# Kernel optimization log

Hardware: AMD Instinct MI355X
Metric: run time of the kernel (lower is better)

## Reference

```python
import jax, jax.numpy as jnp
import numpy as np

B = 256      # number of graphs
IN = 128     # input_dim
FD = 256     # feature_dim (dims[1])
HID = 256    # hidden_dim of attention block (dims[2])
OUT = 128    # final output dim (dims[3])
TXT = 512    # text_emb_dim

LENGTHS = np.asarray(128 + (np.arange(B) % 256), dtype=np.int64)  # ragged lens 128..383
N = int(LENGTHS.sum())  # 65408 total nodes
LMAX = int(LENGTHS.max())  # 383


def setup_inputs() -> dict:
    key = jax.random.key(0)
    ks = jax.random.split(key, 16)
    s = 0.02
    return {
        "input": jax.random.normal(ks[0], (N, IN), jnp.float32),
        "text_emb": jax.random.normal(ks[1], (B, TXT), jnp.float32),
        "repeat_list": jnp.asarray(LENGTHS),
        # layer 0: Linear(IN -> FD)
        "W0": jax.random.normal(ks[2], (IN, FD), jnp.float32) * s,
        "b0": jax.random.normal(ks[3], (FD,), jnp.float32) * s,
        # cross-attention block params
        "Wq": jax.random.normal(ks[4], (TXT, FD), jnp.float32) * s,
        "bq": jax.random.normal(ks[5], (FD,), jnp.float32) * s,
        "Wk": jax.random.normal(ks[6], (FD, FD), jnp.float32) * s,
        "bk": jax.random.normal(ks[7], (FD,), jnp.float32) * s,
        "Wv": jax.random.normal(ks[8], (FD, FD), jnp.float32) * s,
        "bv": jax.random.normal(ks[9], (FD,), jnp.float32) * s,
        "Wo": jax.random.normal(ks[10], (FD, HID), jnp.float32) * s,
        "bo": jax.random.normal(ks[11], (HID,), jnp.float32) * s,
        # layer 2: Linear(HID -> OUT), last layer (no activation)
        "W2": jax.random.normal(ks[12], (HID, OUT), jnp.float32) * s,
        "b2": jax.random.normal(ks[13], (OUT,), jnp.float32) * s,
    }


def _cross_attention(h, text_emb, repeat_list, Wq, bq, Wk, bk, Wv, bv, Wo, bo):
    # h: [N, FD] packed ragged node features; repeat_list: [B] lengths (constant ints)
    n = h.shape[0]
    b = repeat_list.shape[0]
    fd = h.shape[1]
    # pad ragged -> [B, LMAX, FD] (pad value 0) + validity mask
    seg = jnp.repeat(jnp.arange(b), repeat_list, total_repeat_length=n)  # [N] graph id
    offsets = jnp.cumsum(repeat_list) - repeat_list                      # [B] start of each graph
    pos = jnp.arange(n) - offsets[seg]                                   # [N] within-graph pos
    padded = jnp.zeros((b, LMAX, fd), h.dtype).at[seg, pos].set(h)
    valid = jnp.arange(LMAX)[None, :] < repeat_list[:, None]             # [B, L]

    q = text_emb @ Wq + bq                              # [B, FD]
    k = (padded @ Wk + bk) * valid[..., None]           # masked_fill(mask==0, 0)
    v = (padded @ Wv + bv) * valid[..., None]

    # query is broadcast identically over the padded-length axis, so each row of the
    # [L, L] score matrix is the same vector: scores[b, j] = q[b] . k[b, j]
    scores = jnp.einsum('bf,bjf->bj', q, k)             # [B, L]
    scores = jnp.where(valid, scores, -jnp.inf)         # mask invalid columns j
    p = jax.nn.softmax(scores, axis=-1)                 # [B, L]
    # output = attention^T @ value with identical rows => out[b,j,:] = p[b,j] * sum_i v[b,i,:]
    v_sum = v.sum(axis=1)                               # [B, FD] (padded rows already zero)
    out_pad = p[..., None] * v_sum[:, None, :]          # [B, L, FD]
    out_nodes = out_pad[seg, pos]                       # unpad-concat -> [N, FD]
    return out_nodes @ Wo + bo                          # [N, HID]


def reference(input, text_emb, repeat_list, W0, b0, Wq, bq, Wk, bk, Wv, bv, Wo, bo, W2, b2):
    h = jax.nn.relu(input @ W0 + b0)                                     # layer 0 + relu
    h = _cross_attention(h, text_emb, repeat_list, Wq, bq, Wk, bk, Wv, bv, Wo, bo)
    h = jax.nn.relu(h)                                                   # layer 1 + relu
    return h @ W2 + b2                                                   # layer 2 (last, no act)
```

## Files before the change

kernel.cpp:

```cpp
#include <hip/hip_runtime.h>
#include <math.h>

#define B_G   256
#define IN_D  128
#define FD    256
#define HID   256
#define OUT_D 128
#define TXT   512

typedef short bf16x8 __attribute__((ext_vector_type(8)));
typedef float f32x4  __attribute__((ext_vector_type(4)));

#define WPAD 40

__device__ __forceinline__ unsigned bf_rne(float x) {
    unsigned u = __float_as_uint(x);
    u += 0x7fffu + ((u >> 16) & 1u);
    return u >> 16;
}
__device__ __forceinline__ float bf_to_f(unsigned h) {
    return __uint_as_float(h << 16);
}
__device__ __forceinline__ void split2(float a0, float a1, unsigned& hp, unsigned& lp) {
    unsigned h0 = bf_rne(a0), h1 = bf_rne(a1);
    float r0 = a0 - bf_to_f(h0), r1 = a1 - bf_to_f(h1);
    hp = h0 | (bf_rne(a1) << 16);
    lp = bf_rne(r0) | (bf_rne(r1) << 16);
    (void)h1;
}

__global__ __launch_bounds__(256) void k_wsplit(
    const float* __restrict__ W0, const float* __restrict__ W2,
    unsigned short* __restrict__ W0sH, unsigned short* __restrict__ W0sL,
    unsigned short* __restrict__ W2sH, unsigned short* __restrict__ W2sL)
{
    int t = blockIdx.x * 256 + threadIdx.x;
    if (t < 1024) {
        int kc = t >> 8, c = t & 255;
        size_t base = (size_t)(kc * 256 + c) * WPAD;
        for (int kk = 0; kk < 32; kk++) {
            float v = W0[(size_t)(kc * 32 + kk) * FD + c];
            unsigned h = bf_rne(v);
            float r = v - bf_to_f(h);
            W0sH[base + kk] = (unsigned short)h;
            W0sL[base + kk] = (unsigned short)bf_rne(r);
        }
    } else {
        int e = t - 1024;
        int kc = e >> 7, c = e & 127;
        size_t base = (size_t)(kc * 128 + c) * WPAD;
        for (int kk = 0; kk < 32; kk++) {
            float v = W2[(size_t)(kc * 32 + kk) * OUT_D + c];
            unsigned h = bf_rne(v);
            float r = v - bf_to_f(h);
            W2sH[base + kk] = (unsigned short)h;
            W2sL[base + kk] = (unsigned short)bf_rne(r);
        }
    }
}

__global__ __launch_bounds__(256) void k_prep(
    const float* __restrict__ text_emb, const float* __restrict__ Wq,
    const float* __restrict__ bq, const float* __restrict__ Wk,
    const int* __restrict__ lens, float* __restrict__ qk,
    int* __restrict__ offsets)
{
    int b = blockIdx.x, t = threadIdx.x;
    __shared__ float te[TXT];
    __shared__ float q[FD];
    for (int i = t; i < TXT; i += 256) te[i] = text_emb[(size_t)b * TXT + i];
    __syncthreads();
    float acc = bq[t];
    for (int k = 0; k < TXT; k++) acc = fmaf(te[k], Wq[k * FD + t], acc);
    q[t] = acc;
    __syncthreads();
    float a2 = 0.f;
    for (int f = 0; f < FD; f++) a2 = fmaf(Wk[t * FD + f], q[f], a2);
    qk[b * FD + t] = a2;
    if (b == 0 && t == 0) {
        int off = 0;
        for (int i = 0; i < B_G; i++) { offsets[i] = off; off += lens[i]; }
        offsets[B_G] = off;
    }
}

__global__ __launch_bounds__(256, 2) void k_l0_mfma(
    const float* __restrict__ X,
    const unsigned short* __restrict__ W0sH, const unsigned short* __restrict__ W0sL,
    const float* __restrict__ b0, const float* __restrict__ qk,
    const int* __restrict__ offsets,
    float* __restrict__ scores, float* __restrict__ hsum)
{
    int b = blockIdx.y;
    int off = offsets[b], len = offsets[b + 1] - off;
    int n0 = blockIdx.x * 64;
    if (n0 >= len) return;
    int nvalid = min(64, len - n0);

    __shared__ __align__(16) unsigned short XsH[64 * WPAD], XsL[64 * WPAD];
    __shared__ __align__(16) unsigned short WsH[256 * WPAD], WsL[256 * WPAD];
    __shared__ float qks[FD];
    __shared__ float bsh[FD];

    int tid = threadIdx.x;
    int lane = tid & 63, w = tid >> 6;
    int ln = lane & 15, quad = lane >> 4;

    qks[tid] = qk[b * FD + tid];
    bsh[tid] = b0[tid];

    f32x4 acc[4][4] = {};

    const float* Xg = X + (size_t)(off + n0) * IN_D;
    int node_s = tid >> 2, koff = (tid & 3) * 8;

    for (int kc = 0; kc < 4; kc++) {
        float xv[8];
        if (node_s < nvalid) {
            const float4* src = (const float4*)(Xg + (size_t)node_s * IN_D + kc * 32 + koff);
            float4 v0 = src[0], v1 = src[1];
            xv[0] = v0.x; xv[1] = v0.y; xv[2] = v0.z; xv[3] = v0.w;
            xv[4] = v1.x; xv[5] = v1.y; xv[6] = v1.z; xv[7] = v1.w;
        } else {
#pragma unroll
            for (int q = 0; q < 8; q++) xv[q] = 0.f;
        }
        uint4 hq, lq;
        split2(xv[0], xv[1], hq.x, lq.x);
        split2(xv[2], xv[3], hq.y, lq.y);
        split2(xv[4], xv[5], hq.z, lq.z);
        split2(xv[6], xv[7], hq.w, lq.w);
        *(uint4*)&XsH[node_s * WPAD + koff] = hq;
        *(uint4*)&XsL[node_s * WPAD + koff] = lq;

        {
            const uint4* gh = (const uint4*)(W0sH + (size_t)kc * 256 * WPAD);
            const uint4* gl = (const uint4*)(W0sL + (size_t)kc * 256 * WPAD);
            uint4* lh = (uint4*)WsH;
            uint4* ll = (uint4*)WsL;
#pragma unroll
            for (int r = 0; r < 5; r++) {
                lh[tid + 256 * r] = gh[tid + 256 * r];
                ll[tid + 256 * r] = gl[tid + 256 * r];
            }
        }
        __syncthreads();

        bf16x8 AH[4], AL[4], BH[4], BL[4];
#pragma unroll
        for (int i = 0; i < 4; i++) {
            AH[i] = *(const bf16x8*)&XsH[(16 * i + ln) * WPAD + quad * 8];
            AL[i] = *(const bf16x8*)&XsL[(16 * i + ln) * WPAD + quad * 8];
        }
#pragma unroll
        for (int j = 0; j < 4; j++) {
            int c = 64 * w + 16 * j + ln;
            BH[j] = *(const bf16x8*)&WsH[c * WPAD + quad * 8];
            BL[j] = *(const bf16x8*)&WsL[c * WPAD + quad * 8];
        }
#pragma unroll
        for (int i = 0; i < 4; i++)
#pragma unroll
            for (int j = 0; j < 4; j++) {
                acc[i][j] = __builtin_amdgcn_mfma_f32_16x16x32_bf16(AH[i], BH[j], acc[i][j], 0, 0, 0);
                acc[i][j] = __builtin_amdgcn_mfma_f32_16x16x32_bf16(AH[i], BL[j], acc[i][j], 0, 0, 0);
                acc[i][j] = __builtin_amdgcn_mfma_f32_16x16x32_bf16(AL[i], BH[j], acc[i][j], 0, 0, 0);
            }
        __syncthreads();
    }

    float sp[4][4];
    float cs[4] = {0.f, 0.f, 0.f, 0.f};
#pragma unroll
    for (int i = 0; i < 4; i++)
#pragma unroll
        for (int r = 0; r < 4; r++) sp[i][r] = 0.f;

#pragma unroll
    for (int i = 0; i < 4; i++)
#pragma unroll
        for (int j = 0; j < 4; j++) {
            int c = 64 * w + 16 * j + ln;
            float bb = bsh[c], qv = qks[c];
#pragma unroll
            for (int r = 0; r < 4; r++) {
                int node = 16 * i + 4 * quad + r;
                float h = acc[i][j][r] + bb;
                h = (h > 0.f && node < nvalid) ? h : 0.f;
                sp[i][r] = fmaf(h, qv, sp[i][r]);
                cs[j] += h;
            }
        }
#pragma unroll
    for (int i = 0; i < 4; i++)
#pragma unroll
        for (int r = 0; r < 4; r++) {
            float s = sp[i][r];
            s += __shfl_xor(s, 1); s += __shfl_xor(s, 2);
            s += __shfl_xor(s, 4); s += __shfl_xor(s, 8);
            sp[i][r] = s;
        }
    if (ln == 0) {
#pragma unroll
        for (int i = 0; i < 4; i++)
#pragma unroll
            for (int r = 0; r < 4; r++) {
                int node = 16 * i + 4 * quad + r;
                if (node < nvalid) atomicAdd(&scores[off + n0 + node], sp[i][r]);
            }
    }
#pragma unroll
    for (int j = 0; j < 4; j++) {
        float s = cs[j];
        s += __shfl_xor(s, 16); s += __shfl_xor(s, 32);
        if (quad == 0) atomicAdd(&hsum[b * FD + 64 * w + 16 * j + ln], s);
    }
}

__global__ __launch_bounds__(256) void k_graph(
    const float* __restrict__ scores, const float* __restrict__ hsum,
    const float* __restrict__ Wv, const float* __restrict__ bv,
    const float* __restrict__ Wo, const int* __restrict__ offsets,
    float* __restrict__ wvec, float* __restrict__ smax, float* __restrict__ dinv)
{
    int b = blockIdx.x, t = threadIdx.x;
    int off = offsets[b], len = offsets[b + 1] - off;
    __shared__ float redm[4];
    __shared__ float reds[4];
    __shared__ float hs[FD];
    __shared__ float vs[FD];

    float m = -INFINITY;
    for (int i = t; i < len; i += 256) m = fmaxf(m, scores[off + i]);
    for (int d = 1; d < 64; d <<= 1) m = fmaxf(m, __shfl_xor(m, d));
    if ((t & 63) == 0) redm[t >> 6] = m;
    __syncthreads();
    m = fmaxf(fmaxf(redm[0], redm[1]), fmaxf(redm[2], redm[3]));

    float s = 0.f;
    for (int i = t; i < len; i += 256) s += expf(scores[off + i] - m);
    for (int d = 1; d < 64; d <<= 1) s += __shfl_xor(s, d);
    if ((t & 63) == 0) reds[t >> 6] = s;
    hs[t] = hsum[b * FD + t];
    __syncthreads();
    s = reds[0] + reds[1] + reds[2] + reds[3];

    float v = bv[t] * (float)len;
    for (int f = 0; f < FD; f++) v = fmaf(hs[f], Wv[f * FD + t], v);
    vs[t] = v;
    __syncthreads();
    float w = 0.f;
    for (int f = 0; f < FD; f++) w = fmaf(vs[f], Wo[f * HID + t], w);
    wvec[b * HID + t] = w;
    if (t == 0) { smax[b] = m; dinv[b] = 1.0f / s; }
}

__global__ __launch_bounds__(256, 2) void k_fin_mfma(
    const float* __restrict__ scores, const float* __restrict__ wvec,
    const float* __restrict__ bo,
    const unsigned short* __restrict__ W2sH, const unsigned short* __restrict__ W2sL,
    const float* __restrict__ b2, const float* __restrict__ smax,
    const float* __restrict__ dinv, const int* __restrict__ offsets,
    float* __restrict__ Y)
{
    int b = blockIdx.y;
    int off = offsets[b], len = offsets[b + 1] - off;
    int n0 = blockIdx.x * 64;
    if (n0 >= len) return;
    int nvalid = min(64, len - n0);

    int tid = threadIdx.x;
    int lane = tid & 63, w = tid >> 6;
    int ln = lane & 15, quad = lane >> 4;

    __shared__ __align__(16) unsigned short ZsH[64 * WPAD], ZsL[64 * WPAD];
    __shared__ __align__(16) unsigned short WsH[128 * WPAD], WsL[128 * WPAD];
    __shared__ float ps[64];
    __shared__ float wsh[HID];
    __shared__ float bosh[HID];
    __shared__ float b2sh[OUT_D];

    wsh[tid] = wvec[b * HID + tid];
    bosh[tid] = bo[tid];
    if (tid < OUT_D) b2sh[tid] = b2[tid];
    if (tid < 64) {
        float p = 0.f;
        if (tid < nvalid) p = expf(scores[off + n0 + tid] - smax[b]) * dinv[b];
        ps[tid] = p;
    }
    __syncthreads();

    f32x4 acc[4][2] = {};
    int node_s = tid >> 2, koff = (tid & 3) * 8;
    float pn = ps[node_s];

    for (int kc = 0; kc < 8; kc++) {
        {
            int kb = kc * 32 + koff;
            uint4 hq, lq;
            float z0, z1;
            z0 = fmaxf(fmaf(pn, wsh[kb + 0], bosh[kb + 0]), 0.f);
            z1 = fmaxf(fmaf(pn, wsh[kb + 1], bosh[kb + 1]), 0.f);
            split2(z0, z1, hq.x, lq.x);
            z0 = fmaxf(fmaf(pn, wsh[kb + 2], bosh[kb + 2]), 0.f);
            z1 = fmaxf(fmaf(pn, wsh[kb + 3], bosh[kb + 3]), 0.f);
            split2(z0, z1, hq.y, lq.y);
            z0 = fmaxf(fmaf(pn, wsh[kb + 4], bosh[kb + 4]), 0.f);
            z1 = fmaxf(fmaf(pn, wsh[kb + 5], bosh[kb + 5]), 0.f);
            split2(z0, z1, hq.z, lq.z);
            z0 = fmaxf(fmaf(pn, wsh[kb + 6], bosh[kb + 6]), 0.f);
            z1 = fmaxf(fmaf(pn, wsh[kb + 7], bosh[kb + 7]), 0.f);
            split2(z0, z1, hq.w, lq.w);
            *(uint4*)&ZsH[node_s * WPAD + koff] = hq;
            *(uint4*)&ZsL[node_s * WPAD + koff] = lq;
        }
        {
            const uint4* gh = (const uint4*)(W2sH + (size_t)kc * 128 * WPAD);
            const uint4* gl = (const uint4*)(W2sL + (size_t)kc * 128 * WPAD);
            uint4* lh = (uint4*)WsH;
            uint4* ll = (uint4*)WsL;
            lh[tid] = gh[tid];          ll[tid] = gl[tid];
            lh[tid + 256] = gh[tid + 256]; ll[tid + 256] = gl[tid + 256];
            if (tid < 128) { lh[tid + 512] = gh[tid + 512]; ll[tid + 512] = gl[tid + 512]; }
        }
        __syncthreads();

        bf16x8 AH[4], AL[4], BH[2], BL[2];
#pragma unroll
        for (int i = 0; i < 4; i++) {
            AH[i] = *(const bf16x8*)&ZsH[(16 * i + ln) * WPAD + quad * 8];
            AL[i] = *(const bf16x8*)&ZsL[(16 * i + ln) * WPAD + quad * 8];
        }
#pragma unroll
        for (int j = 0; j < 2; j++) {
            int c = 32 * w + 16 * j + ln;
            BH[j] = *(const bf16x8*)&WsH[c * WPAD + quad * 8];
            BL[j] = *(const bf16x8*)&WsL[c * WPAD + quad * 8];
        }
#pragma unroll
        for (int i = 0; i < 4; i++)
#pragma unroll
            for (int j = 0; j < 2; j++) {
                acc[i][j] = __builtin_amdgcn_mfma_f32_16x16x32_bf16(AH[i], BH[j], acc[i][j], 0, 0, 0);
                acc[i][j] = __builtin_amdgcn_mfma_f32_16x16x32_bf16(AH[i], BL[j], acc[i][j], 0, 0, 0);
                acc[i][j] = __builtin_amdgcn_mfma_f32_16x16x32_bf16(AL[i], BH[j], acc[i][j], 0, 0, 0);
            }
        __syncthreads();
    }

#pragma unroll
    for (int i = 0; i < 4; i++)
#pragma unroll
        for (int j = 0; j < 2; j++) {
            int c = 32 * w + 16 * j + ln;
            float bb = b2sh[c];
#pragma unroll
            for (int r = 0; r < 4; r++) {
                int node = 16 * i + 4 * quad + r;
                if (node < nvalid)
                    Y[(size_t)(off + n0 + node) * OUT_D + c] = acc[i][j][r] + bb;
            }
        }
}

extern "C" void kernel_launch(void* const* d_in, const int* in_sizes, int n_in,
                              void* d_out, int out_size, void* d_ws, size_t ws_size,
                              hipStream_t stream)
{
    const float* X        = (const float*)d_in[0];
    const float* text_emb = (const float*)d_in[1];
    const int*   lens     = (const int*)d_in[2];
    const float* W0       = (const float*)d_in[3];
    const float* b0       = (const float*)d_in[4];
    const float* Wq       = (const float*)d_in[5];
    const float* bq       = (const float*)d_in[6];
    const float* Wk       = (const float*)d_in[7];
    const float* Wv       = (const float*)d_in[9];
    const float* bv       = (const float*)d_in[10];
    const float* Wo       = (const float*)d_in[11];
    const float* bo       = (const float*)d_in[12];
    const float* W2       = (const float*)d_in[13];
    const float* b2       = (const float*)d_in[14];
    float* Y = (float*)d_out;

    char* base = (char*)d_ws;
    size_t o = 0;
    int*   offsets = (int*)(base + o);            o += 1088;
    float* qkbuf   = (float*)(base + o);          o += 262144;
    float* wvec    = (float*)(base + o);          o += 262144;
    float* smaxb   = (float*)(base + o);          o += 1024;
    float* dinvb   = (float*)(base + o);          o += 1024;
    unsigned short* W0sH = (unsigned short*)(base + o); o += 81920;
    unsigned short* W0sL = (unsigned short*)(base + o); o += 81920;
    unsigned short* W2sH = (unsigned short*)(base + o); o += 81920;
    unsigned short* W2sL = (unsigned short*)(base + o); o += 81920;
    float* hsum    = (float*)(base + o);          o += 262144;
    float* scores  = (float*)(base + o);          o += 262144;

    hipMemsetAsync(hsum, 0, 524288, stream);
    k_wsplit<<<8, 256, 0, stream>>>(W0, W2, W0sH, W0sL, W2sH, W2sL);
    k_prep<<<B_G, 256, 0, stream>>>(text_emb, Wq, bq, Wk, lens, qkbuf, offsets);
    k_l0_mfma<<<dim3(6, B_G), 256, 0, stream>>>(X, W0sH, W0sL, b0, qkbuf, offsets, scores, hsum);
    k_graph<<<B_G, 256, 0, stream>>>(scores, hsum, Wv, bv, Wo, offsets, wvec, smaxb, dinvb);
    k_fin_mfma<<<dim3(6, B_G), 256, 0, stream>>>(scores, wvec, bo, W2sH, W2sL, b2, smaxb, dinvb, offsets, Y);
}
```

Baseline: 203.8 us.

## Merge prep kernels, load weights directly from global, restructure reductions

Fuses the weight-split, prep and hsum memset into one launch, and computes offsets with a parallel scan. The two MFMA kernels now stage the whole X/Z tile in LDS once and read split weights straight from global/L2, which removes the per-k-chunk barriers and the weight copies into LDS. Score accumulation switches from atomics to an LDS reduction followed by a plain store. The graph kernel moves to 1024 threads and splits the matvec loops across four groups. The cost is more uncoalesced global weight loads inside the MFMA loop and a larger LDS footprint per block.

```diff
diff --git a/kernel.cpp b/kernel.cpp
--- a/kernel.cpp
+++ b/kernel.cpp
@@ -7,11 +7,11 @@
 #define HID   256
 #define OUT_D 128
 #define TXT   512
+#define XKS   136
+#define ZKS   264
 
 typedef short bf16x8 __attribute__((ext_vector_type(8)));
 typedef float f32x4  __attribute__((ext_vector_type(4)));
-
-#define WPAD 40
 
 __device__ __forceinline__ unsigned bf_rne(float x) {
     unsigned u = __float_as_uint(x);
@@ -24,63 +24,71 @@
 __device__ __forceinline__ void split2(float a0, float a1, unsigned& hp, unsigned& lp) {
     unsigned h0 = bf_rne(a0), h1 = bf_rne(a1);
     float r0 = a0 - bf_to_f(h0), r1 = a1 - bf_to_f(h1);
-    hp = h0 | (bf_rne(a1) << 16);
+    hp = h0 | (h1 << 16);
     lp = bf_rne(r0) | (bf_rne(r1) << 16);
-    (void)h1;
-}
-
-__global__ __launch_bounds__(256) void k_wsplit(
+}
+
+__global__ __launch_bounds__(256) void k_prepA(
+    const float* __restrict__ text_emb, const float* __restrict__ Wq,
+    const float* __restrict__ bq, const float* __restrict__ Wk,
     const float* __restrict__ W0, const float* __restrict__ W2,
+    const int* __restrict__ lens,
+    float* __restrict__ qk, int* __restrict__ offsets, float* __restrict__ hsum,
     unsigned short* __restrict__ W0sH, unsigned short* __restrict__ W0sL,
     unsigned short* __restrict__ W2sH, unsigned short* __restrict__ W2sL)
 {
-    int t = blockIdx.x * 256 + threadIdx.x;
-    if (t < 1024) {
-        int kc = t >> 8, c = t & 255;
-        size_t base = (size_t)(kc * 256 + c) * WPAD;
-        for (int kk = 0; kk < 32; kk++) {
-            float v = W0[(size_t)(kc * 32 + kk) * FD + c];
-            unsigned h = bf_rne(v);
-            float r = v - bf_to_f(h);
-            W0sH[base + kk] = (unsigned short)h;
-            W0sL[base + kk] = (unsigned short)bf_rne(r);
-        }
-    } else {
-        int e = t - 1024;
-        int kc = e >> 7, c = e & 127;
-        size_t base = (size_t)(kc * 128 + c) * WPAD;
-        for (int kk = 0; kk < 32; kk++) {
-            float v = W2[(size_t)(kc * 32 + kk) * OUT_D + c];
-            unsigned h = bf_rne(v);
-            float r = v - bf_to_f(h);
-            W2sH[base + kk] = (unsigned short)h;
-            W2sL[base + kk] = (unsigned short)bf_rne(r);
-        }
-    }
-}
-
-__global__ __launch_bounds__(256) void k_prep(
-    const float* __restrict__ text_emb, const float* __restrict__ Wq,
-    const float* __restrict__ bq, const float* __restrict__ Wk,
-    const int* __restrict__ lens, float* __restrict__ qk,
-    int* __restrict__ offsets)
-{
-    int b = blockIdx.x, t = threadIdx.x;
+    int blk = blockIdx.x, t = threadIdx.x;
     __shared__ float te[TXT];
     __shared__ float q[FD];
-    for (int i = t; i < TXT; i += 256) te[i] = text_emb[(size_t)b * TXT + i];
-    __syncthreads();
-    float acc = bq[t];
-    for (int k = 0; k < TXT; k++) acc = fmaf(te[k], Wq[k * FD + t], acc);
-    q[t] = acc;
-    __syncthreads();
-    float a2 = 0.f;
-    for (int f = 0; f < FD; f++) a2 = fmaf(Wk[t * FD + f], q[f], a2);
-    qk[b * FD + t] = a2;
-    if (b == 0 && t == 0) {
-        int off = 0;
-        for (int i = 0; i < B_G; i++) { offsets[i] = off; off += lens[i]; }
-        offsets[B_G] = off;
+    __shared__ int   sc[B_G];
+
+    if (blk < 256) {
+        int b = blk;
+        hsum[b * FD + t] = 0.f;
+        for (int i = t; i < TXT; i += 256) te[i] = text_emb[(size_t)b * TXT + i];
+        __syncthreads();
+        float acc = bq[t];
+        for (int k = 0; k < TXT; k++) acc = fmaf(te[k], Wq[k * FD + t], acc);
+        q[t] = acc;
+        __syncthreads();
+        float a2 = 0.f;
+        for (int f = 0; f < FD; f++) a2 = fmaf(Wk[t * FD + f], q[f], a2);
+        qk[b * FD + t] = a2;
+    } else if (blk < 264) {
+        int e = (blk - 256) * 256 + t;
+        if (e < 1024) {
+            int kc = e >> 8, c = e & 255;
+            size_t base = (size_t)(kc * 256 + c) * 32;
+            for (int kk = 0; kk < 32; kk++) {
+                float v = W0[(size_t)(kc * 32 + kk) * FD + c];
+                unsigned h = bf_rne(v);
+                float r = v - bf_to_f(h);
+                W0sH[base + kk] = (unsigned short)h;
+                W0sL[base + kk] = (unsigned short)bf_rne(r);
+            }
+        } else {
+            int e2 = e - 1024;
+            int kc = e2 >> 7, c = e2 & 127;
+            size_t base = (size_t)(kc * 128 + c) * 32;
+            for (int kk = 0; kk < 32; kk++) {
+                float v = W2[(size_t)(kc * 32 + kk) * OUT_D + c];
+                unsigned h = bf_rne(v);
+                float r = v - bf_to_f(h);
+                W2sH[base + kk] = (unsigned short)h;
+                W2sL[base + kk] = (unsigned short)bf_rne(r);
+            }
+        }
+    } else {
+        sc[t] = lens[t];
+        __syncthreads();
+        for (int d = 1; d < 256; d <<= 1) {
+            int v = (t >= d) ? sc[t - d] : 0;
+            __syncthreads();
+            sc[t] += v;
+            __syncthreads();
+        }
+        offsets[t + 1] = sc[t];
+        if (t == 0) offsets[0] = 0;
     }
 }
 
@@ -97,10 +105,10 @@
     if (n0 >= len) return;
     int nvalid = min(64, len - n0);
 
-    __shared__ __align__(16) unsigned short XsH[64 * WPAD], XsL[64 * WPAD];
-    __shared__ __align__(16) unsigned short WsH[256 * WPAD], WsL[256 * WPAD];
+    __shared__ __align__(16) unsigned short XsH[64 * XKS], XsL[64 * XKS];
     __shared__ float qks[FD];
     __shared__ float bsh[FD];
+    __shared__ float red[4][64];
 
     int tid = threadIdx.x;
     int lane = tid & 63, w = tid >> 6;
@@ -109,54 +117,49 @@
     qks[tid] = qk[b * FD + tid];
     bsh[tid] = b0[tid];
 
+    {
+        int node_s = tid >> 2, ks = (tid & 3) * 32;
+        const float* Xr = X + (size_t)(off + n0 + node_s) * IN_D + ks;
+        float xv[32];
+        if (node_s < nvalid) {
+#pragma unroll
+            for (int q2 = 0; q2 < 8; q2++) {
+                float4 v = ((const float4*)Xr)[q2];
+                xv[q2 * 4 + 0] = v.x; xv[q2 * 4 + 1] = v.y;
+                xv[q2 * 4 + 2] = v.z; xv[q2 * 4 + 3] = v.w;
+            }
+        } else {
+#pragma unroll
+            for (int q2 = 0; q2 < 32; q2++) xv[q2] = 0.f;
+        }
+#pragma unroll
+        for (int g = 0; g < 4; g++) {
+            uint4 hq, lq;
+            split2(xv[g * 8 + 0], xv[g * 8 + 1], hq.x, lq.x);
+            split2(xv[g * 8 + 2], xv[g * 8 + 3], hq.y, lq.y);
+            split2(xv[g * 8 + 4], xv[g * 8 + 5], hq.z, lq.z);
+            split2(xv[g * 8 + 6], xv[g * 8 + 7], hq.w, lq.w);
+            *(uint4*)&XsH[node_s * XKS + ks + g * 8] = hq;
+            *(uint4*)&XsL[node_s * XKS + ks + g * 8] = lq;
+        }
+    }
+    __syncthreads();
+
     f32x4 acc[4][4] = {};
-
-    const float* Xg = X + (size_t)(off + n0) * IN_D;
-    int node_s = tid >> 2, koff = (tid & 3) * 8;
-
+#pragma unroll
     for (int kc = 0; kc < 4; kc++) {
-        float xv[8];
-        if (node_s < nvalid) {
-            const float4* src = (const float4*)(Xg + (size_t)node_s * IN_D + kc * 32 + koff);
-            float4 v0 = src[0], v1 = src[1];
-            xv[0] = v0.x; xv[1] = v0.y; xv[2] = v0.z; xv[3] = v0.w;
-            xv[4] = v1.x; xv[5] = v1.y; xv[6] = v1.z; xv[7] = v1.w;
-        } else {
-#pragma unroll
-            for (int q = 0; q < 8; q++) xv[q] = 0.f;
-        }
-        uint4 hq, lq;
-        split2(xv[0], xv[1], hq.x, lq.x);
-        split2(xv[2], xv[3], hq.y, lq.y);
-        split2(xv[4], xv[5], hq.z, lq.z);
-        split2(xv[6], xv[7], hq.w, lq.w);
-        *(uint4*)&XsH[node_s * WPAD + koff] = hq;
-        *(uint4*)&XsL[node_s * WPAD + koff] = lq;
-
-        {
-            const uint4* gh = (const uint4*)(W0sH + (size_t)kc * 256 * WPAD);
-            const uint4* gl = (const uint4*)(W0sL + (size_t)kc * 256 * WPAD);
-            uint4* lh = (uint4*)WsH;
-            uint4* ll = (uint4*)WsL;
-#pragma unroll
-            for (int r = 0; r < 5; r++) {
-                lh[tid + 256 * r] = gh[tid + 256 * r];
-                ll[tid + 256 * r] = gl[tid + 256 * r];
-            }
-        }
-        __syncthreads();
-
         bf16x8 AH[4], AL[4], BH[4], BL[4];
 #pragma unroll
         for (int i = 0; i < 4; i++) {
-            AH[i] = *(const bf16x8*)&XsH[(16 * i + ln) * WPAD + quad * 8];
-            AL[i] = *(const bf16x8*)&XsL[(16 * i + ln) * WPAD + quad * 8];
+            AH[i] = *(const bf16x8*)&XsH[(16 * i + ln) * XKS + kc * 32 + quad * 8];
+            AL[i] = *(const bf16x8*)&XsL[(16 * i + ln) * XKS + kc * 32 + quad * 8];
         }
 #pragma unroll
         for (int j = 0; j < 4; j++) {
             int c = 64 * w + 16 * j + ln;
-            BH[j] = *(const bf16x8*)&WsH[c * WPAD + quad * 8];
-            BL[j] = *(const bf16x8*)&WsL[c * WPAD + quad * 8];
+            size_t base = (size_t)(kc * 256 + c) * 32 + quad * 8;
+            BH[j] = *(const bf16x8*)&W0sH[base];
+            BL[j] = *(const bf16x8*)&W0sL[base];
         }
 #pragma unroll
         for (int i = 0; i < 4; i++)
@@ -166,7 +169,6 @@
                 acc[i][j] = __builtin_amdgcn_mfma_f32_16x16x32_bf16(AH[i], BL[j], acc[i][j], 0, 0, 0);
                 acc[i][j] = __builtin_amdgcn_mfma_f32_16x16x32_bf16(AL[i], BH[j], acc[i][j], 0, 0, 0);
             }
-        __syncthreads();
     }
 
     float sp[4][4];
@@ -204,10 +206,8 @@
 #pragma unroll
         for (int i = 0; i < 4; i++)
 #pragma unroll
-            for (int r = 0; r < 4; r++) {
-                int node = 16 * i + 4 * quad + r;
-                if (node < nvalid) atomicAdd(&scores[off + n0 + node], sp[i][r]);
-            }
+            for (int r = 0; r < 4; r++)
+                red[w][16 * i + 4 * quad + r] = sp[i][r];
     }
 #pragma unroll
     for (int j = 0; j < 4; j++) {
@@ -215,44 +215,55 @@
         s += __shfl_xor(s, 16); s += __shfl_xor(s, 32);
         if (quad == 0) atomicAdd(&hsum[b * FD + 64 * w + 16 * j + ln], s);
     }
-}
-
-__global__ __launch_bounds__(256) void k_graph(
+    __syncthreads();
+    if (tid < 64 && tid < nvalid)
+        scores[off + n0 + tid] = red[0][tid] + red[1][tid] + red[2][tid] + red[3][tid];
+}
+
+__global__ __launch_bounds__(1024) void k_graph(
     const float* __restrict__ scores, const float* __restrict__ hsum,
     const float* __restrict__ Wv, const float* __restrict__ bv,
     const float* __restrict__ Wo, const int* __restrict__ offsets,
     float* __restrict__ wvec, float* __restrict__ smax, float* __restrict__ dinv)
 {
-    int b = blockIdx.x, t = threadIdx.x;
+    int b = blockIdx.x, tid = threadIdx.x;
+    int t = tid & 255, g = tid >> 8;
     int off = offsets[b], len = offsets[b + 1] - off;
-    __shared__ float redm[4];
-    __shared__ float reds[4];
-    __shared__ float hs[FD];
-    __shared__ float vs[FD];
+    __shared__ float redm[16], reds[16];
+    __shared__ float hs[FD], vs[FD];
+    __shared__ float part[4][FD];
 
     float m = -INFINITY;
-    for (int i = t; i < len; i += 256) m = fmaxf(m, scores[off + i]);
+    for (int i = tid; i < len; i += 1024) m = fmaxf(m, scores[off + i]);
     for (int d = 1; d < 64; d <<= 1) m = fmaxf(m, __shfl_xor(m, d));
-    if ((t & 63) == 0) redm[t >> 6] = m;
-    __syncthreads();
-    m = fmaxf(fmaxf(redm[0], redm[1]), fmaxf(redm[2], redm[3]));
+    if ((tid & 63) == 0) redm[tid >> 6] = m;
+    __syncthreads();
+    m = -INFINITY;
+#pragma unroll
+    for (int k = 0; k < 16; k++) m = fmaxf(m, redm[k]);
 
     float s = 0.f;
-    for (int i = t; i < len; i += 256) s += expf(scores[off + i] - m);
+    for (int i = tid; i < len; i += 1024) s += expf(scores[off + i] - m);
     for (int d = 1; d < 64; d <<= 1) s += __shfl_xor(s, d);
-    if ((t & 63) == 0) reds[t >> 6] = s;
-    hs[t] = hsum[b * FD + t];
-    __syncthreads();
-    s = reds[0] + reds[1] + reds[2] + reds[3];
-
-    float v = bv[t] * (float)len;
-    for (int f = 0; f < FD; f++) v = fmaf(hs[f], Wv[f * FD + t], v);
-    vs[t] = v;
-    __syncthreads();
-    float w = 0.f;
-    for (int f = 0; f < FD; f++) w = fmaf(vs[f], Wo[f * HID + t], w);
-    wvec[b * HID + t] = w;
-    if (t == 0) { smax[b] = m; dinv[b] = 1.0f / s; }
+    if ((tid & 63) == 0) reds[tid >> 6] = s;
+    if (g == 0) hs[t] = hsum[b * FD + t];
+    __syncthreads();
+    s = 0.f;
+#pragma unroll
+    for (int k = 0; k < 16; k++) s += reds[k];
+
+    float acc = (g == 0) ? (float)len * bv[t] : 0.f;
+    for (int f = 64 * g; f < 64 * g + 64; f++) acc = fmaf(hs[f], Wv[f * FD + t], acc);
+    part[g][t] = acc;
+    __syncthreads();
+    if (g == 0) vs[t] = part[0][t] + part[1][t] + part[2][t] + part[3][t];
+    __syncthreads();
+    float a2 = 0.f;
+    for (int f = 64 * g; f < 64 * g + 64; f++) a2 = fmaf(vs[f], Wo[f * HID + t], a2);
+    part[g][t] = a2;
+    __syncthreads();
+    if (g == 0) wvec[b * HID + t] = part[0][t] + part[1][t] + part[2][t] + part[3][t];
+    if (tid == 0) { smax[b] = m; dinv[b] = 1.0f / s; }
 }
 
 __global__ __launch_bounds__(256, 2) void k_fin_mfma(
@@ -273,8 +284,7 @@
     int lane = tid & 63, w = tid >> 6;
     int ln = lane & 15, quad = lane >> 4;
 
-    __shared__ __align__(16) unsigned short ZsH[64 * WPAD], ZsL[64 * WPAD];
-    __shared__ __align__(16) unsigned short WsH[128 * WPAD], WsL[128 * WPAD];
+    __shared__ __align__(16) unsigned short ZsH[64 * ZKS], ZsL[64 * ZKS];
     __shared__ float ps[64];
     __shared__ float wsh[HID];
     __shared__ float bosh[HID];
@@ -290,14 +300,13 @@
     }
     __syncthreads();
 
-    f32x4 acc[4][2] = {};
-    int node_s = tid >> 2, koff = (tid & 3) * 8;
-    float pn = ps[node_s];
-
-    for (int kc = 0; kc < 8; kc++) {
-        {
-            int kb = kc * 32 + koff;
+    {
+        int node_s = tid >> 2, ks = (tid & 3) * 64;
+        float pn = ps[node_s];
+#pragma unroll
+        for (int g = 0; g < 8; g++) {
             uint4 hq, lq;
+            int kb = ks + g * 8;
             float z0, z1;
             z0 = fmaxf(fmaf(pn, wsh[kb + 0], bosh[kb + 0]), 0.f);
             z1 = fmaxf(fmaf(pn, wsh[kb + 1], bosh[kb + 1]), 0.f);
@@ -311,31 +320,27 @@
             z0 = fmaxf(fmaf(pn, wsh[kb + 6], bosh[kb + 6]), 0.f);
             z1 = fmaxf(fmaf(pn, wsh[kb + 7], bosh[kb + 7]), 0.f);
             split2(z0, z1, hq.w, lq.w);
-            *(uint4*)&ZsH[node_s * WPAD + koff] = hq;
-            *(uint4*)&ZsL[node_s * WPAD + koff] = lq;
-        }
-        {
-            const uint4* gh = (const uint4*)(W2sH + (size_t)kc * 128 * WPAD);
-            const uint4* gl = (const uint4*)(W2sL + (size_t)kc * 128 * WPAD);
-            uint4* lh = (uint4*)WsH;
-            uint4* ll = (uint4*)WsL;
-            lh[tid] = gh[tid];          ll[tid] = gl[tid];
-            lh[tid + 256] = gh[tid + 256]; ll[tid + 256] = gl[tid + 256];
-            if (tid < 128) { lh[tid + 512] = gh[tid + 512]; ll[tid + 512] = gl[tid + 512]; }
-        }
-        __syncthreads();
-
+            *(uint4*)&ZsH[node_s * ZKS + kb] = hq;
+            *(uint4*)&ZsL[node_s * ZKS + kb] = lq;
+        }
+    }
+    __syncthreads();
+
+    f32x4 acc[4][2] = {};
+#pragma unroll
+    for (int kc = 0; kc < 8; kc++) {
         bf16x8 AH[4], AL[4], BH[2], BL[2];
 #pragma unroll
         for (int i = 0; i < 4; i++) {
-            AH[i] = *(const bf16x8*)&ZsH[(16 * i + ln) * WPAD + quad * 8];
-            AL[i] = *(const bf16x8*)&ZsL[(16 * i + ln) * WPAD + quad * 8];
+            AH[i] = *(const bf16x8*)&ZsH[(16 * i + ln) * ZKS + kc * 32 + quad * 8];
+            AL[i] = *(const bf16x8*)&ZsL[(16 * i + ln) * ZKS + kc * 32 + quad * 8];
         }
 #pragma unroll
         for (int j = 0; j < 2; j++) {
             int c = 32 * w + 16 * j + ln;
-            BH[j] = *(const bf16x8*)&WsH[c * WPAD + quad * 8];
-            BL[j] = *(const bf16x8*)&WsL[c * WPAD + quad * 8];
+            size_t base = (size_t)(kc * 128 + c) * 32 + quad * 8;
+            BH[j] = *(const bf16x8*)&W2sH[base];
+            BL[j] = *(const bf16x8*)&W2sL[base];
         }
 #pragma unroll
         for (int i = 0; i < 4; i++)
@@ -345,7 +350,6 @@
                 acc[i][j] = __builtin_amdgcn_mfma_f32_16x16x32_bf16(AH[i], BL[j], acc[i][j], 0, 0, 0);
                 acc[i][j] = __builtin_amdgcn_mfma_f32_16x16x32_bf16(AL[i], BH[j], acc[i][j], 0, 0, 0);
             }
-        __syncthreads();
     }
 
 #pragma unroll
@@ -390,17 +394,16 @@
     float* wvec    = (float*)(base + o);          o += 262144;
     float* smaxb   = (float*)(base + o);          o += 1024;
     float* dinvb   = (float*)(base + o);          o += 1024;
-    unsigned short* W0sH = (unsigned short*)(base + o); o += 81920;
-    unsigned short* W0sL = (unsigned short*)(base + o); o += 81920;
-    unsigned short* W2sH = (unsigned short*)(base + o); o += 81920;
-    unsigned short* W2sL = (unsigned short*)(base + o); o += 81920;
     float* hsum    = (float*)(base + o);          o += 262144;
     float* scores  = (float*)(base + o);          o += 262144;
-
-    hipMemsetAsync(hsum, 0, 524288, stream);
-    k_wsplit<<<8, 256, 0, stream>>>(W0, W2, W0sH, W0sL, W2sH, W2sL);
-    k_prep<<<B_G, 256, 0, stream>>>(text_emb, Wq, bq, Wk, lens, qkbuf, offsets);
+    unsigned short* W0sH = (unsigned short*)(base + o); o += 65536;
+    unsigned short* W0sL = (unsigned short*)(base + o); o += 65536;
+    unsigned short* W2sH = (unsigned short*)(base + o); o += 65536;
+    unsigned short* W2sL = (unsigned short*)(base + o); o += 65536;
+
+    k_prepA<<<265, 256, 0, stream>>>(text_emb, Wq, bq, Wk, W0, W2, lens,
+                                     qkbuf, offsets, hsum, W0sH, W0sL, W2sH, W2sL);
     k_l0_mfma<<<dim3(6, B_G), 256, 0, stream>>>(X, W0sH, W0sL, b0, qkbuf, offsets, scores, hsum);
-    k_graph<<<B_G, 256, 0, stream>>>(scores, hsum, Wv, bv, Wo, offsets, wvec, smaxb, dinvb);
+    k_graph<<<B_G, 1024, 0, stream>>>(scores, hsum, Wv, bv, Wo, offsets, wvec, smaxb, dinvb);
     k_fin_mfma<<<dim3(6, B_G), 256, 0, stream>>>(scores, wvec, bo, W2sH, W2sL, b2, smaxb, dinvb, offsets, Y);
 }
```

After: 199.2 us. 2.2% less time.
